# Kernel optimization log

Measured on AMD Instinct MI355X. Metric: run time of the kernel, lower is better.

The kernel has to match this reference:

```python
import jax, jax.numpy as jnp
import numpy as np


def _conv1x1_relu(x, w, b):
    # x: [B,C,H,W], w: [O,C], b: [O] -> relu(1x1 conv) [B,O,H,W]
    y = jnp.einsum('oc,bchw->bohw', w, x) + b[None, :, None, None]
    return jax.nn.relu(y)


def setup_inputs() -> dict:
    key = jax.random.key(0)
    ks = jax.random.split(key, 9)
    B, C, H, W = 16, 128, 256, 64
    s = 1.0 / np.sqrt(C)
    return {
        'rep': jax.random.normal(ks[0], (B, C, H, W), jnp.float32),
        'wq': jax.random.normal(ks[1], (C, C), jnp.float32) * s,
        'bq': jax.random.normal(ks[2], (C,), jnp.float32) * 0.02,
        'wk': jax.random.normal(ks[3], (C, C), jnp.float32) * s,
        'bk': jax.random.normal(ks[4], (C,), jnp.float32) * 0.02,
        'wv': jax.random.normal(ks[5], (C, C), jnp.float32) * s,
        'bv': jax.random.normal(ks[6], (C,), jnp.float32) * 0.02,
        'wfc': jax.random.normal(ks[7], (C, C), jnp.float32) * s,
        'bfc': jax.random.normal(ks[8], (C,), jnp.float32) * 0.02,
    }


def reference(rep, wq, bq, wk, bk, wv, bv, wfc, bfc):
    C = rep.shape[1]
    # ReLU-activated 1x1-conv Q/K/V projections, then permute to [B,W,H,C]
    q = _conv1x1_relu(rep, wq, bq).transpose(0, 3, 2, 1)  # [B,W,H,C]
    k = _conv1x1_relu(rep, wk, bk).transpose(0, 3, 2, 1)
    v = _conv1x1_relu(rep, wv, bv).transpose(0, 3, 2, 1)
    # attention over the H axis, independently per (B, W)
    attn = jnp.einsum('bwhc,bwgc->bwhg', q, k) / jnp.sqrt(jnp.asarray(C, q.dtype))
    attn = jax.nn.softmax(attn, axis=-1)  # [B,W,H,H]
    out = jnp.einsum('bwhg,bwgc->bwhc', attn, v)  # [B,W,H,C]
    # back to NCHW, final ReLU 1x1 conv
    out = out.transpose(0, 3, 2, 1)  # [B,C,H,W]
    return _conv1x1_relu(out, wfc, bfc)
```

## Files before the change

### kernel.cpp

```cpp
#include <hip/hip_runtime.h>


typedef __attribute__((ext_vector_type(8))) short short8;
typedef __attribute__((ext_vector_type(4))) float f32x4;

#define MFMA16(acc, a, b) (acc) = __builtin_amdgcn_mfma_f32_16x16x32_bf16((a), (b), (acc), 0, 0, 0)

__device__ __forceinline__ unsigned short f2b(float f) {
  unsigned u = __builtin_bit_cast(unsigned, f);
  u = (u + 0x7fffu + ((u >> 16) & 1u)) >> 16;
  return (unsigned short)u;
}

__device__ __forceinline__ unsigned adr_s(int r, int c) {
  return (unsigned)(((r << 8) + (c << 1)) ^ ((r & 7) << 4));
}
__device__ __forceinline__ unsigned adr_q(int r, int c) {
  return (unsigned)(((r << 8) + (c << 1)) ^ (((r ^ (r >> 3)) & 7) << 4));
}
__device__ __forceinline__ unsigned adr_vt(int c, int g) {
  unsigned blk = (unsigned)(((g >> 3) ^ (c & 7) ^ ((c >> 3) & 7)) & 31);
  return (unsigned)((c << 9) + (blk << 4) + ((g & 7) << 1));
}
__device__ __forceinline__ unsigned ps_adr(int r, int c) {
  return (unsigned)(((r << 7) + (c << 1)) ^ (((r ^ (r >> 3)) & 7) << 4));
}

__device__ __forceinline__ short8 ldsf(const char* p, unsigned off) {
  return *(const short8*)(p + off);
}

__global__ __launch_bounds__(256) void k0_wcvt(
    const float* __restrict__ wq, const float* __restrict__ wk,
    const float* __restrict__ wv, const float* __restrict__ wfc,
    unsigned short* __restrict__ wb)
{
  int i = blockIdx.x * 256 + threadIdx.x;
  int mat = i >> 12, off = (i & 4095) * 4;
  const float* src = (mat == 0) ? wq : (mat == 1) ? wk : (mat == 2) ? wv : wfc;
  float4 v = *(const float4*)(src + off);
  uint2 u;
  u.x = (unsigned)f2b(v.x) | ((unsigned)f2b(v.y) << 16);
  u.y = (unsigned)f2b(v.z) | ((unsigned)f2b(v.w) << 16);
  *(uint2*)(wb + mat * 16384 + off) = u;
}


__device__ __forceinline__ void k1_one(const unsigned short* wmat, const float* bias,
    unsigned short* dst, const char* XS, char* WS,
    int brel, int n0, int wvid, int l, int l16, int g4) {
  const int strip = wvid * 16;
  short8 wf[4];
#pragma unroll
  for (int kk = 0; kk < 4; ++kk)
    wf[kk] = *(const short8*)(wmat + (strip + l16) * 128 + kk * 32 + g4 * 8);
  float bv4[4];
#pragma unroll
  for (int r = 0; r < 4; ++r) bv4[r] = bias[strip + g4 * 4 + r];

  f32x4 acc[8];
#pragma unroll
  for (int nt = 0; nt < 8; ++nt) acc[nt] = (f32x4){0.f, 0.f, 0.f, 0.f};
#pragma unroll
  for (int nt = 0; nt < 8; ++nt) {
#pragma unroll
    for (int kk = 0; kk < 4; ++kk) {
      short8 xb = ldsf(XS, adr_q(nt * 16 + l16, kk * 32 + g4 * 8));
      MFMA16(acc[nt], wf[kk], xb);
    }
  }
#pragma unroll
  for (int hf = 0; hf < 2; ++hf) {
    __syncthreads();
#pragma unroll
    for (int nt4 = 0; nt4 < 4; ++nt4) {
      int nt = hf * 4 + nt4;
      float y0 = fmaxf(acc[nt][0] + bv4[0], 0.f);
      float y1 = fmaxf(acc[nt][1] + bv4[1], 0.f);
      float y2 = fmaxf(acc[nt][2] + bv4[2], 0.f);
      float y3 = fmaxf(acc[nt][3] + bv4[3], 0.f);
      uint2 u;
      u.x = (unsigned)f2b(y0) | ((unsigned)f2b(y1) << 16);
      u.y = (unsigned)f2b(y2) | ((unsigned)f2b(y3) << 16);
      int row = nt4 * 16 + l16;
      unsigned cb = (unsigned)(wvid * 32 + g4 * 8);
      *(uint2*)(WS + (unsigned)(row << 8) + (cb ^ ((unsigned)(row & 7) << 4))) = u;
    }
    __syncthreads();
#pragma unroll
    for (int it = 0; it < 8; ++it) {
      int row = it * 8 + wvid;
      unsigned u = *(const unsigned*)(WS + (unsigned)(row << 8) +
                                     (((unsigned)(l << 2)) ^ ((unsigned)(row & 7) << 4)));
      int n = n0 + hf * 64 + row;
      int h = n >> 6, w = n & 63;
      ((unsigned*)dst)[(size_t)((brel * 64 + w) * 256 + h) * 64 + l] = u;
    }
  }
}

__global__ __launch_bounds__(512, 4) void k1_qkv(
    const float* __restrict__ rep, const unsigned short* __restrict__ wb,
    const float* __restrict__ bq, const float* __restrict__ bk,
    const float* __restrict__ bv,
    unsigned short* __restrict__ qo, unsigned short* __restrict__ ko,
    unsigned short* __restrict__ vo, int b0)
{
  extern __shared__ char smem[];
  char* XS = smem;
  char* WS = smem + (32 << 10);

  const int t = threadIdx.x;
  const int wvid = t >> 6, l = t & 63, l16 = l & 15, g4 = l >> 4;
  const int brel = blockIdx.x >> 7;
  const int n0 = (blockIdx.x & 127) * 128;
  const int b = b0 + brel;

#pragma unroll
  for (int it = 0; it < 8; ++it) {
    int i = it * 512 + t;
    int c = i >> 5, j4 = i & 31;
    float4 xv = *(const float4*)(rep + (size_t)(b * 128 + c) * 16384 + n0 + j4 * 4);
    float vv[4] = {xv.x, xv.y, xv.z, xv.w};
#pragma unroll
    for (int r = 0; r < 4; ++r)
      *(unsigned short*)(XS + adr_q(j4 * 4 + r, c)) = f2b(vv[r]);
  }
  __syncthreads();

  k1_one(wb,         bq, qo, XS, WS, brel, n0, wvid, l, l16, g4);
  k1_one(wb + 16384, bk, ko, XS, WS, brel, n0, wvid, l, l16, g4);
  k1_one(wb + 32768, bv, vo, XS, WS, brel, n0, wvid, l, l16, g4);
}


__global__ __launch_bounds__(1024, 1) void k2_attn(
    const unsigned short* __restrict__ qws, const unsigned short* __restrict__ kws,
    const unsigned short* __restrict__ vws, unsigned short* __restrict__ aws)
{
  extern __shared__ char smem[];
  char* KS  = smem;
  char* VTS = smem + (64 << 10);

  const int t = threadIdx.x;
  const int wvid = t >> 6, l = t & 63, l16 = l & 15, g4 = l >> 4;
  char* PS = smem + (128 << 10) + (wvid << 11);

  const int brel = blockIdx.x >> 6;
  const int w = blockIdx.x & 63;
  const size_t wbase = (size_t)((brel * 64 + w)) * 256;

  const int hb = wvid * 16;

  short8 qa[4];
#pragma unroll
  for (int kk = 0; kk < 4; ++kk)
    qa[kk] = *(const short8*)(qws + (wbase + hb + l16) * 128 + kk * 32 + g4 * 8);

#pragma unroll
  for (int it = 0; it < 4; ++it) {
    int i = it * 1024 + t;
    int g = i >> 4, c16 = i & 15;
    short8 kv = *(const short8*)(kws + (wbase + g) * 128 + c16 * 8);
    *(short8*)(KS + adr_s(g, c16 * 8)) = kv;
  }
#pragma unroll
  for (int it = 0; it < 4; ++it) {
    int i = it * 1024 + t;
    int g = i >> 4, c16 = i & 15;
    short8 vv = *(const short8*)(vws + (wbase + g) * 128 + c16 * 8);
#pragma unroll
    for (int j = 0; j < 8; ++j)
      *(unsigned short*)(VTS + adr_vt(c16 * 8 + j, g)) = (unsigned short)vv[j];
  }
  __syncthreads();

  const float SCL2 = 0.08838834764831845f * 1.4426950408889634f;

  f32x4 sc[16];
#pragma unroll
  for (int gt = 0; gt < 16; ++gt) {
    f32x4 acc = {0.f, 0.f, 0.f, 0.f};
#pragma unroll
    for (int kk = 0; kk < 4; ++kk) {
      short8 kb = ldsf(KS, adr_s(gt * 16 + l16, kk * 32 + g4 * 8));
      MFMA16(acc, qa[kk], kb);
    }
    sc[gt] = acc;
  }
  float mx[4], rcps[4];
#pragma unroll
  for (int r = 0; r < 4; ++r) {
    float mm = sc[0][r];
#pragma unroll
    for (int gt = 1; gt < 16; ++gt) mm = fmaxf(mm, sc[gt][r]);
    mm = fmaxf(mm, __shfl_xor(mm, 1, 64));
    mm = fmaxf(mm, __shfl_xor(mm, 2, 64));
    mm = fmaxf(mm, __shfl_xor(mm, 4, 64));
    mm = fmaxf(mm, __shfl_xor(mm, 8, 64));
    mx[r] = mm;
  }
#pragma unroll
  for (int gt = 0; gt < 16; ++gt)
#pragma unroll
    for (int r = 0; r < 4; ++r)
      sc[gt][r] = exp2f((sc[gt][r] - mx[r]) * SCL2);
#pragma unroll
  for (int r = 0; r < 4; ++r) {
    float s = 0.f;
#pragma unroll
    for (int gt = 0; gt < 16; ++gt) s += sc[gt][r];
    s += __shfl_xor(s, 1, 64);
    s += __shfl_xor(s, 2, 64);
    s += __shfl_xor(s, 4, 64);
    s += __shfl_xor(s, 8, 64);
    rcps[r] = 1.0f / s;
  }

  f32x4 oacc[8];
#pragma unroll
  for (int nt = 0; nt < 8; ++nt) oacc[nt] = (f32x4){0.f, 0.f, 0.f, 0.f};
#pragma unroll
  for (int gh = 0; gh < 4; ++gh) {
#pragma unroll
    for (int gt4 = 0; gt4 < 4; ++gt4) {
      int gt = gh * 4 + gt4;
      int gc = gt4 * 16 + l16;
#pragma unroll
      for (int r = 0; r < 4; ++r)
        *(unsigned short*)(PS + ps_adr(g4 * 4 + r, gc)) = f2b(sc[gt][r]);
    }
#pragma unroll
    for (int kk2 = 0; kk2 < 2; ++kk2) {
      short8 pa = ldsf(PS, ps_adr(l16, kk2 * 32 + g4 * 8));
#pragma unroll
      for (int nt = 0; nt < 8; ++nt) {
        short8 vb = ldsf(VTS, adr_vt(nt * 16 + l16, gh * 64 + kk2 * 32 + g4 * 8));
        MFMA16(oacc[nt], pa, vb);
      }
    }
  }

#pragma unroll
  for (int ch = 0; ch < 2; ++ch) {
#pragma unroll
    for (int nt4 = 0; nt4 < 4; ++nt4) {
      int nt = ch * 4 + nt4;
#pragma unroll
      for (int r = 0; r < 4; ++r)
        *(unsigned short*)(PS + ps_adr(g4 * 4 + r, nt4 * 16 + l16)) =
            f2b(oacc[nt][r] * rcps[r]);
    }
#pragma unroll
    for (int it = 0; it < 8; ++it) {
      int row = it * 2 + (l >> 5);
      int cd  = l & 31;
      unsigned base = (unsigned)(row << 7) +
          (((unsigned)(cd << 2)) ^ (((unsigned)((row ^ (row >> 3)) & 7)) << 4));
      unsigned lo = *(const unsigned short*)(PS + base);
      unsigned hi = *(const unsigned short*)(PS + base + 2);
      ((unsigned*)aws)[(wbase + hb + row) * 64 + ch * 32 + cd] = lo | (hi << 16);
    }
  }
}


__global__ __launch_bounds__(512, 4) void k3_conv(
    const unsigned short* __restrict__ aws, const unsigned short* __restrict__ wb,
    const float* __restrict__ bfc, float* __restrict__ out, int b0)
{
  extern __shared__ char smem[];
  char* AS = smem;

  const int t = threadIdx.x;
  const int wvid = t >> 6, l = t & 63, l16 = l & 15, g4 = l >> 4;
  (void)l;
  const int brel = blockIdx.x >> 6;
  const int n0 = (blockIdx.x & 63) * 256;
  const int b = b0 + brel;

#pragma unroll
  for (int it = 0; it < 8; ++it) {
    int i = it * 512 + t;
    int nn = i >> 4, c16 = i & 15;
    int n = n0 + nn;
    int h = n >> 6, w = n & 63;
    short8 av = *(const short8*)(aws + ((size_t)((brel * 64 + w) * 256 + h)) * 128 + c16 * 8);
    *(short8*)(AS + adr_s(nn, c16 * 8)) = av;
  }
  __syncthreads();

  const int strip = wvid * 16;
  const unsigned short* wfcb = wb + 3 * 16384;
  short8 wf[4];
#pragma unroll
  for (int kk = 0; kk < 4; ++kk)
    wf[kk] = *(const short8*)(wfcb + (strip + l16) * 128 + kk * 32 + g4 * 8);
  float bv4[4];
#pragma unroll
  for (int r = 0; r < 4; ++r) bv4[r] = bfc[strip + g4 * 4 + r];

#pragma unroll
  for (int nt = 0; nt < 16; ++nt) {
    f32x4 acc = {0.f, 0.f, 0.f, 0.f};
#pragma unroll
    for (int kk = 0; kk < 4; ++kk) {
      short8 ab = ldsf(AS, adr_s(nt * 16 + l16, kk * 32 + g4 * 8));
      MFMA16(acc, wf[kk], ab);
    }
#pragma unroll
    for (int r = 0; r < 4; ++r) {
      int o = strip + g4 * 4 + r;
      out[(size_t)(b * 128 + o) * 16384 + n0 + nt * 16 + l16] = fmaxf(acc[r] + bv4[r], 0.f);
    }
  }
}

extern "C" void kernel_launch(void* const* d_in, const int* in_sizes, int n_in,
                              void* d_out, int out_size, void* d_ws, size_t ws_size,
                              hipStream_t stream) {
  const float* rep = (const float*)d_in[0];
  const float* wq  = (const float*)d_in[1];
  const float* bq  = (const float*)d_in[2];
  const float* wk  = (const float*)d_in[3];
  const float* bk  = (const float*)d_in[4];
  const float* wv  = (const float*)d_in[5];
  const float* bv  = (const float*)d_in[6];
  const float* wfc = (const float*)d_in[7];
  const float* bfc = (const float*)d_in[8];
  float* out = (float*)d_out;
  (void)in_sizes; (void)n_in; (void)out_size;

  hipFuncSetAttribute((const void*)k1_qkv,  hipFuncAttributeMaxDynamicSharedMemorySize, 48 * 1024);
  hipFuncSetAttribute((const void*)k2_attn, hipFuncAttributeMaxDynamicSharedMemorySize, 160 * 1024);
  hipFuncSetAttribute((const void*)k3_conv, hipFuncAttributeMaxDynamicSharedMemorySize, 64 * 1024);

  const size_t wb_bytes = 4 * 16384 * 2;
  const size_t per_b = (size_t)16384 * 128 * 2;
  if (ws_size < wb_bytes + 4 * per_b) return;
  size_t nb_max = (ws_size - wb_bytes) / (4 * per_b);
  int nb = (int)(nb_max < 16 ? nb_max : 16);

  char* ws = (char*)d_ws;
  unsigned short* qws = (unsigned short*)(ws);
  unsigned short* kws = (unsigned short*)(ws + (size_t)nb * per_b);
  unsigned short* vws = (unsigned short*)(ws + (size_t)nb * per_b * 2);
  unsigned short* aws = (unsigned short*)(ws + (size_t)nb * per_b * 3);
  unsigned short* wb  = (unsigned short*)(ws + (size_t)nb * per_b * 4);

  k0_wcvt<<<dim3(64), dim3(256), 0, stream>>>(wq, wk, wv, wfc, wb);

  for (int b0 = 0; b0 < 16; b0 += nb) {
    int nbc = (16 - b0) < nb ? (16 - b0) : nb;
    k1_qkv<<<dim3(nbc * 128), dim3(512), 48 * 1024, stream>>>(
        rep, wb, bq, bk, bv, qws, kws, vws, b0);
    k2_attn<<<dim3(nbc * 64), dim3(1024), 160 * 1024, stream>>>(qws, kws, vws, aws);
    k3_conv<<<dim3(nbc * 64), dim3(512), 64 * 1024, stream>>>(aws, wb, bfc, out, b0);
  }
}
```

Baseline: 247.9 us.

## Keep softmax probabilities in registers by transposing QK^T MFMA and permuting K rows

The QK^T MFMA operands are swapped so each lane holds one query row's scores. K rows are permuted on their way into shared memory so that the packed bf16 probabilities line up directly with the A-operand layout of the PV MFMA. This removes the per-wave LDS round trip for the probability matrix and cuts the softmax reductions to two cross-lane shuffles. Normalisation now happens before the bf16 rounding of P instead of being applied to the output, which slightly changes numerics and relies on the lane permutation being exactly right.

```diff
diff --git a/kernel.cpp b/kernel.cpp
--- a/kernel.cpp
+++ b/kernel.cpp
@@ -3,6 +3,7 @@
 
 typedef __attribute__((ext_vector_type(8))) short short8;
 typedef __attribute__((ext_vector_type(4))) float f32x4;
+typedef __attribute__((ext_vector_type(4))) int int4v;
 
 #define MFMA16(acc, a, b) (acc) = __builtin_amdgcn_mfma_f32_16x16x32_bf16((a), (b), (acc), 0, 0, 0)
 
@@ -161,8 +162,9 @@
   for (int it = 0; it < 4; ++it) {
     int i = it * 1024 + t;
     int g = i >> 4, c16 = i & 15;
+    int gp = (g & ~31) | ((g & 4) << 2) | ((g >> 1) & 12) | (g & 3);
     short8 kv = *(const short8*)(kws + (wbase + g) * 128 + c16 * 8);
-    *(short8*)(KS + adr_s(g, c16 * 8)) = kv;
+    *(short8*)(KS + adr_s(gp, c16 * 8)) = kv;
   }
 #pragma unroll
   for (int it = 0; it < 4; ++it) {
@@ -184,60 +186,53 @@
 #pragma unroll
     for (int kk = 0; kk < 4; ++kk) {
       short8 kb = ldsf(KS, adr_s(gt * 16 + l16, kk * 32 + g4 * 8));
-      MFMA16(acc, qa[kk], kb);
+      MFMA16(acc, kb, qa[kk]);
     }
     sc[gt] = acc;
   }
-  float mx[4], rcps[4];
-#pragma unroll
-  for (int r = 0; r < 4; ++r) {
-    float mm = sc[0][r];
-#pragma unroll
-    for (int gt = 1; gt < 16; ++gt) mm = fmaxf(mm, sc[gt][r]);
-    mm = fmaxf(mm, __shfl_xor(mm, 1, 64));
-    mm = fmaxf(mm, __shfl_xor(mm, 2, 64));
-    mm = fmaxf(mm, __shfl_xor(mm, 4, 64));
-    mm = fmaxf(mm, __shfl_xor(mm, 8, 64));
-    mx[r] = mm;
-  }
-#pragma unroll
-  for (int gt = 0; gt < 16; ++gt)
-#pragma unroll
-    for (int r = 0; r < 4; ++r)
-      sc[gt][r] = exp2f((sc[gt][r] - mx[r]) * SCL2);
-#pragma unroll
-  for (int r = 0; r < 4; ++r) {
-    float s = 0.f;
-#pragma unroll
-    for (int gt = 0; gt < 16; ++gt) s += sc[gt][r];
-    s += __shfl_xor(s, 1, 64);
-    s += __shfl_xor(s, 2, 64);
-    s += __shfl_xor(s, 4, 64);
-    s += __shfl_xor(s, 8, 64);
-    rcps[r] = 1.0f / s;
+
+  float mm = fmaxf(fmaxf(sc[0][0], sc[0][1]), fmaxf(sc[0][2], sc[0][3]));
+#pragma unroll
+  for (int gt = 1; gt < 16; ++gt) {
+    float m4 = fmaxf(fmaxf(sc[gt][0], sc[gt][1]), fmaxf(sc[gt][2], sc[gt][3]));
+    mm = fmaxf(mm, m4);
+  }
+  mm = fmaxf(mm, __shfl_xor(mm, 16, 64));
+  mm = fmaxf(mm, __shfl_xor(mm, 32, 64));
+  const float mneg = -mm * SCL2;
+  float s = 0.f;
+#pragma unroll
+  for (int gt = 0; gt < 16; ++gt) {
+#pragma unroll
+    for (int r = 0; r < 4; ++r) {
+      float p = exp2f(fmaf(sc[gt][r], SCL2, mneg));
+      sc[gt][r] = p;
+      s += p;
+    }
+  }
+  s += __shfl_xor(s, 16, 64);
+  s += __shfl_xor(s, 32, 64);
+  const float rcp = 1.0f / s;
+
+  unsigned pk0[16], pk1[16];
+#pragma unroll
+  for (int gt = 0; gt < 16; ++gt) {
+    pk0[gt] = (unsigned)f2b(sc[gt][0] * rcp) | ((unsigned)f2b(sc[gt][1] * rcp) << 16);
+    pk1[gt] = (unsigned)f2b(sc[gt][2] * rcp) | ((unsigned)f2b(sc[gt][3] * rcp) << 16);
   }
 
   f32x4 oacc[8];
 #pragma unroll
   for (int nt = 0; nt < 8; ++nt) oacc[nt] = (f32x4){0.f, 0.f, 0.f, 0.f};
 #pragma unroll
-  for (int gh = 0; gh < 4; ++gh) {
-#pragma unroll
-    for (int gt4 = 0; gt4 < 4; ++gt4) {
-      int gt = gh * 4 + gt4;
-      int gc = gt4 * 16 + l16;
-#pragma unroll
-      for (int r = 0; r < 4; ++r)
-        *(unsigned short*)(PS + ps_adr(g4 * 4 + r, gc)) = f2b(sc[gt][r]);
-    }
-#pragma unroll
-    for (int kk2 = 0; kk2 < 2; ++kk2) {
-      short8 pa = ldsf(PS, ps_adr(l16, kk2 * 32 + g4 * 8));
-#pragma unroll
-      for (int nt = 0; nt < 8; ++nt) {
-        short8 vb = ldsf(VTS, adr_vt(nt * 16 + l16, gh * 64 + kk2 * 32 + g4 * 8));
-        MFMA16(oacc[nt], pa, vb);
-      }
+  for (int kks = 0; kks < 8; ++kks) {
+    int4v pv = {(int)pk0[2 * kks], (int)pk1[2 * kks],
+                (int)pk0[2 * kks + 1], (int)pk1[2 * kks + 1]};
+    short8 pa = __builtin_bit_cast(short8, pv);
+#pragma unroll
+    for (int nt = 0; nt < 8; ++nt) {
+      short8 vb = ldsf(VTS, adr_vt(nt * 16 + l16, kks * 32 + g4 * 8));
+      MFMA16(oacc[nt], pa, vb);
     }
   }
 
@@ -248,8 +243,7 @@
       int nt = ch * 4 + nt4;
 #pragma unroll
       for (int r = 0; r < 4; ++r)
-        *(unsigned short*)(PS + ps_adr(g4 * 4 + r, nt4 * 16 + l16)) =
-            f2b(oacc[nt][r] * rcps[r]);
+        *(unsigned short*)(PS + ps_adr(g4 * 4 + r, nt4 * 16 + l16)) = f2b(oacc[nt][r]);
     }
 #pragma unroll
     for (int it = 0; it < 8; ++it) {
```

After: 234.4 us. 5.5% less time.
